# Kernel optimization log

Measured on AMD Instinct MI355X. Metric: run time of the kernel, lower is better.

## Reference

```python
import jax, jax.numpy as jnp
import numpy as np

B, S, D = 4, 2048, 2048
E = 64           # num_experts
TOPK = 2         # num_experts_per_token


def setup_inputs() -> dict:
    key = jax.random.key(0)
    k1, k2, k3 = jax.random.split(key, 3)
    x_real = jax.random.normal(k1, (B, S, D), dtype=jnp.float32)
    x_imag = jax.random.normal(k2, (B, S, D), dtype=jnp.float32)
    # flax Dense: kernel [in_features, out_features] with lecun_normal-ish scale
    W = jax.random.normal(k3, (2 * D, E), dtype=jnp.float32) / np.sqrt(2.0 * D)
    b = jnp.zeros((E,), dtype=jnp.float32)
    return {"x_real": x_real, "x_imag": x_imag, "W": W, "b": b}


def reference(x_real, x_imag, W, b):
    # amp = |x|, phase = angle(x) for x = x_real + i*x_imag
    amp = jnp.hypot(x_real, x_imag)                 # [B,S,D]
    phase = jnp.arctan2(x_imag, x_real)             # [B,S,D]
    routing_input = jnp.concatenate([amp, phase], axis=-1)  # [B,S,2D]
    scores = jnp.einsum('bsf,fe->bse', routing_input, W) + b  # [B,S,E]
    probs = jax.nn.softmax(scores, axis=-1)
    top_k_probs, top_k_indices = jax.lax.top_k(probs, TOPK)   # [B,S,K]
    top_k_probs = top_k_probs / jnp.sum(top_k_probs, axis=-1, keepdims=True)
    return (top_k_probs, top_k_indices)
```

## Files before the change

### kernel.cpp

```cpp
#include <hip/hip_runtime.h>
#include <math.h>

#define NTOK 8192
#define DD   2048
#define EE   64
#define TSTRIP 16
#define NCH 16
#define PROB_N (NTOK*2)
#define AROW 136
#define F_PSTRIDE (128*4*64*8)

typedef _Float16 f16x8 __attribute__((ext_vector_type(8)));
typedef _Float16 f16x4 __attribute__((ext_vector_type(4)));
typedef float    f32x4 __attribute__((ext_vector_type(4)));

__device__ __forceinline__ float fast_atan2f(float y, float x) {
    const float ax = __builtin_fabsf(x), ay = __builtin_fabsf(y);
    const float hi = fmaxf(ax, ay), lo = fminf(ax, ay);
    const bool  big = lo > 0.4142135679721832f * hi;
    const float num = big ? (lo - hi) : lo;
    const float den = big ? (lo + hi) : hi;
    float rc = __builtin_amdgcn_rcpf(den);
    rc = rc * fmaf(-den, rc, 2.0f);
    const float z  = num * rc;
    const float z2 = z * z;
    float p = fmaf(z2, 8.05374449538e-2f, -1.38776856032e-1f);
    p = fmaf(z2, p, 1.99777106478e-1f);
    p = fmaf(z2, p, -3.33329491539e-1f);
    float r = fmaf(z * z2, p, z);
    r = r + (big ? 0.78539816339744830962f : 0.0f);
    r = (ay > ax) ? (1.57079632679489661923f - r) : r;
    r = (x < 0.0f) ? (3.14159265358979323846f - r) : r;
    return copysignf(r, y);
}

__device__ __forceinline__ void fsplit2(float x, _Float16& h1, _Float16& h2s) {
    const _Float16 a = (_Float16)x;
    h1 = a;
    h2s = (_Float16)((x - (float)a) * 2048.0f);
}

__global__ __launch_bounds__(256) void wsplit(const float* __restrict__ W,
                                              _Float16* __restrict__ F) {
    const int g  = blockIdx.x * 256 + threadIdx.x;
    const int e  = g & 63;
    const int q  = g >> 6;
    const int d0 = q * 4;
    const int nt = e >> 4;
    const int lane = ((d0 & 31) >> 3) * 16 + (e & 15);
    const int j0 = d0 & 7;
    const int cka = 2 * (d0 >> 5);

    f16x4 a1, a2, p1, p2;
    #pragma unroll
    for (int i = 0; i < 4; ++i) {
        _Float16 h, l;
        fsplit2(W[(size_t)(d0 + i) * EE + e], h, l);      a1[i] = h; a2[i] = l;
        fsplit2(W[(size_t)(DD + d0 + i) * EE + e], h, l); p1[i] = h; p2[i] = l;
    }
    *(f16x4*)&F[((size_t)(0 * 128 + cka)     * 4 + nt) * 512 + lane * 8 + j0] = a1;
    *(f16x4*)&F[((size_t)(1 * 128 + cka)     * 4 + nt) * 512 + lane * 8 + j0] = a2;
    *(f16x4*)&F[((size_t)(0 * 128 + cka + 1) * 4 + nt) * 512 + lane * 8 + j0] = p1;
    *(f16x4*)&F[((size_t)(1 * 128 + cka + 1) * 4 + nt) * 512 + lane * 8 + j0] = p2;
}

__global__ __launch_bounds__(512, 4) void gemm_topk(
    const float* __restrict__ xr, const float* __restrict__ xi,
    const _Float16* __restrict__ F, const float* __restrict__ bias,
    float* __restrict__ out)
{
    __shared__ __align__(16) _Float16 A[2][2][2][TSTRIP][AROW];
    __shared__ float scoreH[2][TSTRIP][EE];

    const int tid = threadIdx.x;
    const int t0  = blockIdx.x * TSTRIP;
    const int wv = tid >> 6, lane = tid & 63;
    const int nt = wv & 3, kh = wv >> 2;
    const int fm = lane & 15, fq = lane >> 4;
    const int kh_s  = tid >> 8;
    const int tok_s = (tid >> 4) & 15;
    const int f4    = tid & 15;

    const float bv = bias[lane];

    const float* prx = xr + (size_t)(t0 + tok_s) * DD + kh_s * 1024 + f4 * 4;
    const float* pix = xi + (size_t)(t0 + tok_s) * DD + kh_s * 1024 + f4 * 4;
    const int posa = 64 * (f4 >> 3) + (f4 & 7) * 4;

    auto sprocess = [&](float4 vr, float4 vi, int buf) {
        const float ar[4] = {vr.x, vr.y, vr.z, vr.w};
        const float ai[4] = {vi.x, vi.y, vi.z, vi.w};
        f16x4 a1, a2, p1, p2;
        #pragma unroll
        for (int i = 0; i < 4; ++i) {
            const float amp = __builtin_amdgcn_sqrtf(fmaf(ar[i], ar[i], ai[i] * ai[i]));
            const float ph  = fast_atan2f(ai[i], ar[i]);
            _Float16 h, l;
            fsplit2(amp, h, l); a1[i] = h; a2[i] = l;
            fsplit2(ph,  h, l); p1[i] = h; p2[i] = l;
        }
        *(f16x4*)&A[buf][kh_s][0][tok_s][posa]      = a1;
        *(f16x4*)&A[buf][kh_s][1][tok_s][posa]      = a2;
        *(f16x4*)&A[buf][kh_s][0][tok_s][posa + 32] = p1;
        *(f16x4*)&A[buf][kh_s][1][tok_s][posa + 32] = p2;
    };

    f32x4 accH = (f32x4){0.f, 0.f, 0.f, 0.f};
    f32x4 accL = (f32x4){0.f, 0.f, 0.f, 0.f};

    const _Float16* bbase = F + ((size_t)(kh * 64) * 4 + nt) * 512 + lane * 8;

    f16x8 bh[2][4], bl[2][4];

    {
        const float4 vr0 = *(const float4*)prx;
        const float4 vi0 = *(const float4*)pix;
        #pragma unroll
        for (int j = 0; j < 4; ++j) {
            bh[0][j] = *(const f16x8*)(bbase + j * 2048);
            bl[0][j] = *(const f16x8*)(bbase + F_PSTRIDE + j * 2048);
        }
        sprocess(vr0, vi0, 0);
    }
    asm volatile("s_waitcnt lgkmcnt(0)" ::: "memory");
    __builtin_amdgcn_s_barrier();
    asm volatile("" ::: "memory");

    #pragma unroll
    for (int c = 0; c < NCH; ++c) {
        const int buf  = c & 1;
        const int nbuf = buf ^ 1;
        const bool more = (c + 1 < NCH);
        float4 nvr, nvi;
        if (more) {
            nvr = *(const float4*)(prx + (c + 1) * 64);
            nvi = *(const float4*)(pix + (c + 1) * 64);
            const _Float16* nb = bbase + (size_t)(c + 1) * 8192;
            #pragma unroll
            for (int j = 0; j < 4; ++j) {
                bh[nbuf][j] = *(const f16x8*)(nb + j * 2048);
                bl[nbuf][j] = *(const f16x8*)(nb + F_PSTRIDE + j * 2048);
            }
        }
        #pragma unroll
        for (int j = 0; j < 4; ++j) {
            const f16x8 a1 = *(const f16x8*)&A[buf][kh][0][fm][j * 32 + fq * 8];
            const f16x8 a2 = *(const f16x8*)&A[buf][kh][1][fm][j * 32 + fq * 8];
            accH = __builtin_amdgcn_mfma_f32_16x16x32_f16(a1, bh[buf][j], accH, 0, 0, 0);
            accL = __builtin_amdgcn_mfma_f32_16x16x32_f16(a1, bl[buf][j], accL, 0, 0, 0);
            accL = __builtin_amdgcn_mfma_f32_16x16x32_f16(a2, bh[buf][j], accL, 0, 0, 0);
        }
        if (more) {
            sprocess(nvr, nvi, nbuf);
            asm volatile("s_waitcnt lgkmcnt(0)" ::: "memory");
            __builtin_amdgcn_s_barrier();
            asm volatile("" ::: "memory");
        }
    }

    #pragma unroll
    for (int r = 0; r < 4; ++r)
        scoreH[kh][fq * 4 + r][nt * 16 + fm] = fmaf(accL[r], 4.8828125e-4f, accH[r]);
    __syncthreads();

    #pragma unroll
    for (int rep = 0; rep < 2; ++rep) {
        const int tok = wv * 2 + rep;
        float v1 = scoreH[0][tok][lane] + scoreH[1][tok][lane] + bv;
        float v2 = -INFINITY;
        int   i1 = lane, i2 = 64;
        #pragma unroll
        for (int off = 1; off < 64; off <<= 1) {
            const float ov1 = __shfl_xor(v1, off, 64);
            const int   oi1 = __shfl_xor(i1, off, 64);
            const float ov2 = __shfl_xor(v2, off, 64);
            const int   oi2 = __shfl_xor(i2, off, 64);
            const bool b1 = (ov1 > v1) || (ov1 == v1 && oi1 < i1);
            const float n1 = b1 ? ov1 : v1;  const int ni1 = b1 ? oi1 : i1;
            const float c1 = b1 ? v1  : ov1; const int ci1 = b1 ? i1  : oi1;
            const float c2 = b1 ? ov2 : v2;  const int ci2 = b1 ? oi2 : i2;
            const bool b2 = (c1 > c2) || (c1 == c2 && ci1 < ci2);
            v1 = n1; i1 = ni1;
            v2 = b2 ? c1 : c2; i2 = b2 ? ci1 : ci2;
        }
        if (lane == 0) {
            const int t = t0 + tok;
            const float z  = expf(v2 - v1);
            const float p1 = 1.0f / (1.0f + z);
            const float p2 = z / (1.0f + z);
            out[(size_t)t * 2 + 0] = p1;
            out[(size_t)t * 2 + 1] = p2;
            out[PROB_N + (size_t)t * 2 + 0] = (float)i1;
            out[PROB_N + (size_t)t * 2 + 1] = (float)i2;
        }
    }
}

extern "C" void kernel_launch(void* const* d_in, const int* in_sizes, int n_in,
                              void* d_out, int out_size, void* d_ws, size_t ws_size,
                              hipStream_t stream) {
    const float* xr = (const float*)d_in[0];
    const float* xi = (const float*)d_in[1];
    const float* W  = (const float*)d_in[2];
    const float* b  = (const float*)d_in[3];
    float* out = (float*)d_out;
    _Float16* F = (_Float16*)d_ws;

    wsplit<<<128, 256, 0, stream>>>(W, F);
    gemm_topk<<<NTOK / TSTRIP, 512, 0, stream>>>(xr, xi, F, b, out);
}
```

Baseline: 164.1 us.

## Deepen global load prefetch to two chunks ahead with explicit vmcnt waits

Replaces compiler-scheduled global loads with inline-asm dwordx4 loads and manual s_waitcnt vmcnt counters, so x and weight fragments for chunk c+2 are issued while chunk c is computed. This keeps two chunks of memory requests in flight instead of one, to hide HBM latency in the streaming GEMM. Sched barriers pin the instruction order, which limits compiler scheduling. Correctness now depends on the vmcnt counts matching the number of loads issued.

```diff
diff --git a/kernel.cpp b/kernel.cpp
--- a/kernel.cpp
+++ b/kernel.cpp
@@ -13,6 +13,26 @@
 typedef _Float16 f16x8 __attribute__((ext_vector_type(8)));
 typedef _Float16 f16x4 __attribute__((ext_vector_type(4)));
 typedef float    f32x4 __attribute__((ext_vector_type(4)));
+
+__device__ __forceinline__ f16x8 gload_f16x8(const _Float16* p) {
+    f16x8 r;
+    asm volatile("global_load_dwordx4 %0, %1, off" : "=v"(r) : "v"(p));
+    return r;
+}
+__device__ __forceinline__ f32x4 gload_f32x4(const float* p) {
+    f32x4 r;
+    asm volatile("global_load_dwordx4 %0, %1, off" : "=v"(r) : "v"(p));
+    return r;
+}
+#define VMWAIT(n) do { \
+    asm volatile("s_waitcnt vmcnt(" #n ")" ::: "memory"); \
+    __builtin_amdgcn_sched_barrier(0); \
+} while (0)
+#define LBAR() do { \
+    asm volatile("s_waitcnt lgkmcnt(0)" ::: "memory"); \
+    __builtin_amdgcn_s_barrier(); \
+    __builtin_amdgcn_sched_barrier(0); \
+} while (0)
 
 __device__ __forceinline__ float fast_atan2f(float y, float x) {
     const float ax = __builtin_fabsf(x), ay = __builtin_fabsf(y);
@@ -87,14 +107,12 @@
     const float* pix = xi + (size_t)(t0 + tok_s) * DD + kh_s * 1024 + f4 * 4;
     const int posa = 64 * (f4 >> 3) + (f4 & 7) * 4;
 
-    auto sprocess = [&](float4 vr, float4 vi, int buf) {
-        const float ar[4] = {vr.x, vr.y, vr.z, vr.w};
-        const float ai[4] = {vi.x, vi.y, vi.z, vi.w};
+    auto sprocess = [&](f32x4 vr, f32x4 vi, int buf) {
         f16x4 a1, a2, p1, p2;
         #pragma unroll
         for (int i = 0; i < 4; ++i) {
-            const float amp = __builtin_amdgcn_sqrtf(fmaf(ar[i], ar[i], ai[i] * ai[i]));
-            const float ph  = fast_atan2f(ai[i], ar[i]);
+            const float amp = __builtin_amdgcn_sqrtf(fmaf(vr[i], vr[i], vi[i] * vi[i]));
+            const float ph  = fast_atan2f(vi[i], vr[i]);
             _Float16 h, l;
             fsplit2(amp, h, l); a1[i] = h; a2[i] = l;
             fsplit2(ph,  h, l); p1[i] = h; p2[i] = l;
@@ -111,37 +129,30 @@
     const _Float16* bbase = F + ((size_t)(kh * 64) * 4 + nt) * 512 + lane * 8;
 
     f16x8 bh[2][4], bl[2][4];
-
-    {
-        const float4 vr0 = *(const float4*)prx;
-        const float4 vi0 = *(const float4*)pix;
-        #pragma unroll
-        for (int j = 0; j < 4; ++j) {
-            bh[0][j] = *(const f16x8*)(bbase + j * 2048);
-            bl[0][j] = *(const f16x8*)(bbase + F_PSTRIDE + j * 2048);
-        }
-        sprocess(vr0, vi0, 0);
-    }
-    asm volatile("s_waitcnt lgkmcnt(0)" ::: "memory");
-    __builtin_amdgcn_s_barrier();
-    asm volatile("" ::: "memory");
+    f32x4 xrb[2], xib[2];
+
+    xrb[0] = gload_f32x4(prx);
+    xib[0] = gload_f32x4(pix);
+    #pragma unroll
+    for (int j = 0; j < 4; ++j) {
+        bh[0][j] = gload_f16x8(bbase + j * 2048);
+        bl[0][j] = gload_f16x8(bbase + F_PSTRIDE + j * 2048);
+    }
+    VMWAIT(8);
+    sprocess(xrb[0], xib[0], 0);
+    xrb[1] = gload_f32x4(prx + 64);
+    xib[1] = gload_f32x4(pix + 64);
+    #pragma unroll
+    for (int j = 0; j < 4; ++j) {
+        bh[1][j] = gload_f16x8(bbase + 8192 + j * 2048);
+        bl[1][j] = gload_f16x8(bbase + 8192 + F_PSTRIDE + j * 2048);
+    }
+    LBAR();
 
     #pragma unroll
     for (int c = 0; c < NCH; ++c) {
-        const int buf  = c & 1;
-        const int nbuf = buf ^ 1;
-        const bool more = (c + 1 < NCH);
-        float4 nvr, nvi;
-        if (more) {
-            nvr = *(const float4*)(prx + (c + 1) * 64);
-            nvi = *(const float4*)(pix + (c + 1) * 64);
-            const _Float16* nb = bbase + (size_t)(c + 1) * 8192;
-            #pragma unroll
-            for (int j = 0; j < 4; ++j) {
-                bh[nbuf][j] = *(const f16x8*)(nb + j * 2048);
-                bl[nbuf][j] = *(const f16x8*)(nb + F_PSTRIDE + j * 2048);
-            }
-        }
+        const int buf = c & 1;
+        if (c < NCH - 1) { VMWAIT(10); } else { VMWAIT(0); }
         #pragma unroll
         for (int j = 0; j < 4; ++j) {
             const f16x8 a1 = *(const f16x8*)&A[buf][kh][0][fm][j * 32 + fq * 8];
@@ -150,11 +161,20 @@
             accL = __builtin_amdgcn_mfma_f32_16x16x32_f16(a1, bl[buf][j], accL, 0, 0, 0);
             accL = __builtin_amdgcn_mfma_f32_16x16x32_f16(a2, bh[buf][j], accL, 0, 0, 0);
         }
-        if (more) {
-            sprocess(nvr, nvi, nbuf);
-            asm volatile("s_waitcnt lgkmcnt(0)" ::: "memory");
-            __builtin_amdgcn_s_barrier();
-            asm volatile("" ::: "memory");
+        if (c < NCH - 1) {
+            VMWAIT(8);
+            sprocess(xrb[buf ^ 1], xib[buf ^ 1], buf ^ 1);
+            if (c < NCH - 2) {
+                xrb[buf] = gload_f32x4(prx + (c + 2) * 64);
+                xib[buf] = gload_f32x4(pix + (c + 2) * 64);
+                const _Float16* nb = bbase + (size_t)(c + 2) * 8192;
+                #pragma unroll
+                for (int j = 0; j < 4; ++j) {
+                    bh[buf][j] = gload_f16x8(nb + j * 2048);
+                    bl[buf][j] = gload_f16x8(nb + F_PSTRIDE + j * 2048);
+                }
+            }
+            LBAR();
         }
     }
 
```

Measured after the change: 172.5 us. +5.1%, slower.
